# Performance work log

Hardware: AMD Instinct MI355X
Metric: run time of the kernel (lower is better)

The kernel has to match this reference:

```python
import jax, jax.numpy as jnp
import numpy as np

D_MODEL = 1024
N_HEADS = 16
HEAD_DIM = D_MODEL // N_HEADS
EPS = 1e-6


def _phi(x):
    # elu(x) + 1 feature map
    return jax.nn.elu(x) + 1.0


def setup_inputs() -> dict:
    key = jax.random.key(0)
    ks = jax.random.split(key, 12)
    B, N, M = 4, 4096, 4096
    s = 1.0 / np.sqrt(D_MODEL)
    return {
        "queries": jax.random.normal(ks[0], (B, N, D_MODEL), jnp.float32),
        "keys": jax.random.normal(ks[1], (B, M, D_MODEL), jnp.float32),
        "values": jax.random.normal(ks[2], (B, M, D_MODEL), jnp.float32),
        "wq": jax.random.normal(ks[3], (D_MODEL, D_MODEL), jnp.float32) * s,
        "bq": jax.random.normal(ks[4], (D_MODEL,), jnp.float32) * s,
        "wk": jax.random.normal(ks[5], (D_MODEL, D_MODEL), jnp.float32) * s,
        "bk": jax.random.normal(ks[6], (D_MODEL,), jnp.float32) * s,
        "wv": jax.random.normal(ks[7], (D_MODEL, D_MODEL), jnp.float32) * s,
        "bv": jax.random.normal(ks[8], (D_MODEL,), jnp.float32) * s,
        "wo": jax.random.normal(ks[9], (D_MODEL, D_MODEL), jnp.float32) * s,
        "bo": jax.random.normal(ks[10], (D_MODEL,), jnp.float32) * s,
    }


def reference(queries, keys, values, wq, bq, wk, bk, wv, bv, wo, bo):
    B, N, _ = queries.shape
    M = keys.shape[1]
    H, Dh = N_HEADS, HEAD_DIM
    # projections + head split -> [B, H, seq, Dh]
    q = _phi((queries @ wq.T + bq).reshape(B, N, H, Dh).transpose(0, 2, 1, 3))
    k = _phi((keys @ wk.T + bk).reshape(B, M, H, Dh).transpose(0, 2, 1, 3))
    v = (values @ wv.T + bv).reshape(B, M, H, Dh).transpose(0, 2, 1, 3)
    # kv aggregation: [B,H,Dh,Dh]
    kv = jnp.einsum("bhmd,bhme->bhde", k, v)
    # normalizer: [B,H,Dh]
    z = k.sum(axis=2)
    num = jnp.einsum("bhnd,bhde->bhne", q, kv)
    den = jnp.einsum("bhnd,bhd->bhn", q, z)[..., None] + EPS
    out = (num / den).transpose(0, 2, 1, 3).reshape(B, N, H * Dh)
    return out @ wo.T + bo
```

## Files before the change

### kernel.cpp

```cpp
#include <hip/hip_runtime.h>

#define EPS 1e-6f

typedef __attribute__((ext_vector_type(8))) __bf16 bf16x8;
typedef __attribute__((ext_vector_type(4))) float f32x4;
typedef __attribute__((ext_vector_type(4))) unsigned short us4v;
typedef __attribute__((ext_vector_type(8))) unsigned short us8v;
typedef unsigned short us;

__device__ inline us f2bf(float f) {
  unsigned int u = __builtin_bit_cast(unsigned int, f);
  unsigned int r = (u + 0x7fffu + ((u >> 16) & 1u)) >> 16;
  return (us)r;
}
__device__ inline float bf2f(us s) {
  unsigned int u = ((unsigned int)s) << 16;
  return __builtin_bit_cast(float, u);
}

__device__ inline void gl_lds16(const us* g, us* l) {
  __builtin_amdgcn_global_load_lds(
      (const __attribute__((address_space(1))) unsigned int*)g,
      (__attribute__((address_space(3))) unsigned int*)l, 16, 0, 0);
}

__global__ __launch_bounds__(256) void conv_bf16(const float* __restrict__ s,
                                                 us* __restrict__ d) {
  int idx = blockIdx.x * 256 + threadIdx.x;
  size_t base = (size_t)idx * 8;
  float4 a = *(const float4*)(s + base);
  float4 b = *(const float4*)(s + base + 4);
  us8v o;
  o[0] = f2bf(a.x); o[1] = f2bf(a.y); o[2] = f2bf(a.z); o[3] = f2bf(a.w);
  o[4] = f2bf(b.x); o[5] = f2bf(b.y); o[6] = f2bf(b.z); o[7] = f2bf(b.w);
  *(us8v*)(d + base) = o;
}

__global__ __launch_bounds__(256) void conv_w4(const float* __restrict__ wq,
                                               const float* __restrict__ wk,
                                               const float* __restrict__ wv,
                                               const float* __restrict__ wo,
                                               us* __restrict__ dq,
                                               us* __restrict__ dk,
                                               us* __restrict__ dv,
                                               us* __restrict__ dwo) {
  int bid = blockIdx.x;
  int msel = bid >> 9, lb = bid & 511;
  const float* s = (msel == 0) ? wq : (msel == 1) ? wk : (msel == 2) ? wv : wo;
  us* d = (msel == 0) ? dq : (msel == 1) ? dk : (msel == 2) ? dv : dwo;
  int idx = lb * 256 + threadIdx.x;
  size_t base = (size_t)idx * 8;
  float4 a = *(const float4*)(s + base);
  float4 b = *(const float4*)(s + base + 4);
  us8v o;
  o[0] = f2bf(a.x); o[1] = f2bf(a.y); o[2] = f2bf(a.z); o[3] = f2bf(a.w);
  o[4] = f2bf(b.x); o[5] = f2bf(b.y); o[6] = f2bf(b.z); o[7] = f2bf(b.w);
  *(us8v*)(d + base) = o;
}

template <int MODE>
__global__ __launch_bounds__(512, 2) void proj_gemm(const us* __restrict__ X,
                                                    const us* __restrict__ W,
                                                    const float* __restrict__ bias,
                                                    void* __restrict__ Yv) {
  __shared__ alignas(16) us As[2][256 * 64];
  __shared__ alignas(16) us Bs[2][256 * 64];

  const int t = threadIdx.x;
  const int wave = t >> 6, lane = t & 63;
  const int q4 = lane >> 4, l16 = lane & 15;
  const int wm = wave >> 2, wn = wave & 3;
  const int bid = blockIdx.x;
  const int rowg = (bid & 7) * 8 + (bid >> 5);
  const int colg = (bid >> 3) & 3;
  const int rowBase = rowg << 8;
  const int colBase = colg << 8;

  const int tr = t >> 3;
  const int gsw = ((t & 7) ^ (tr & 7)) * 8;
  const us* Xg = X + (size_t)(rowBase + tr) * 1024 + gsw;
  const us* Wg = W + (size_t)(colBase + tr) * 1024 + gsw;

  const int gx0 = ((0 | q4) ^ (l16 & 7)) * 8;
  const int gx1 = ((4 | q4) ^ (l16 & 7)) * 8;
  const int arow_off = (wm * 128 + l16) * 64;
  const int brow_off = (wn * 64 + l16) * 64;

  f32x4 acc[8][4];
#pragma unroll
  for (int i = 0; i < 8; i++)
#pragma unroll
    for (int j = 0; j < 4; j++) acc[i][j] = (f32x4){0.f, 0.f, 0.f, 0.f};

#define STAGE_A(kt, h)                                                      \
  {                                                                         \
    us* d_ = &As[(kt) & 1][((h) * 128 + wave * 8) * 64];                    \
    const us* s_ = Xg + (size_t)((h) * 128) * 1024 + (kt) * 64;             \
    gl_lds16(s_, d_);                                                       \
    gl_lds16(s_ + (size_t)64 * 1024, d_ + 64 * 64);                         \
  }
#define STAGE_B(kt, h)                                                      \
  {                                                                         \
    us* d_ = &Bs[(kt) & 1][((h) * 128 + wave * 8) * 64];                    \
    const us* s_ = Wg + (size_t)((h) * 128) * 1024 + (kt) * 64;             \
    gl_lds16(s_, d_);                                                       \
    gl_lds16(s_ + (size_t)64 * 1024, d_ + 64 * 64);                         \
  }
#define PH_SYNC_PRE()                                                       \
  asm volatile("s_barrier" ::: "memory");                                   \
  asm volatile("s_waitcnt lgkmcnt(0)" ::: "memory");                        \
  __builtin_amdgcn_sched_barrier(0);                                        \
  __builtin_amdgcn_s_setprio(1);
#define PH_SYNC_POST()                                                      \
  __builtin_amdgcn_s_setprio(0);                                           \
  asm volatile("s_barrier" ::: "memory");
#define MFMA16(J, AF)                                                       \
  _Pragma("unroll") for (int s_i = 0; s_i < 2; ++s_i)                       \
  _Pragma("unroll") for (int ks = 0; ks < 2; ++ks)                          \
  _Pragma("unroll") for (int ni = 0; ni < 4; ++ni)                          \
    acc[2 * (J) + s_i][ni] = __builtin_amdgcn_mfma_f32_16x16x32_bf16(       \
        AF[s_i][ks], bfv[ni][ks], acc[2 * (J) + s_i][ni], 0, 0, 0);

  STAGE_B(0, 0); STAGE_B(0, 1);
  STAGE_A(0, 0); STAGE_A(0, 1);
  STAGE_B(1, 0); STAGE_B(1, 1);
  asm volatile("s_waitcnt vmcnt(4)" ::: "memory");
  asm volatile("s_barrier" ::: "memory");

#pragma unroll 2
  for (int m = 0; m < 16; ++m) {
    const int b = m & 1;
    const us* Ar = &As[b][arow_off];
    const us* Br = &Bs[b][brow_off];
    bf16x8 bfv[4][2];

    {
      bf16x8 af[2][2];
#pragma unroll
      for (int s_i = 0; s_i < 2; ++s_i) {
        af[s_i][0] = *(const bf16x8*)(Ar + (0 + s_i) * 1024 + gx0);
        af[s_i][1] = *(const bf16x8*)(Ar + (0 + s_i) * 1024 + gx1);
      }
#pragma unroll
      for (int ni = 0; ni < 4; ++ni) {
        bfv[ni][0] = *(const bf16x8*)(Br + ni * 1024 + gx0);
        bfv[ni][1] = *(const bf16x8*)(Br + ni * 1024 + gx1);
      }
      if (m < 15) STAGE_A(m + 1, 0);
      PH_SYNC_PRE();
      MFMA16(0, af);
      PH_SYNC_POST();
    }
    {
      bf16x8 af[2][2];
#pragma unroll
      for (int s_i = 0; s_i < 2; ++s_i) {
        af[s_i][0] = *(const bf16x8*)(Ar + (2 + s_i) * 1024 + gx0);
        af[s_i][1] = *(const bf16x8*)(Ar + (2 + s_i) * 1024 + gx1);
      }
      if (m < 15) STAGE_A(m + 1, 1);
      PH_SYNC_PRE();
      MFMA16(1, af);
      PH_SYNC_POST();
    }
    {
      bf16x8 af[2][2];
#pragma unroll
      for (int s_i = 0; s_i < 2; ++s_i) {
        af[s_i][0] = *(const bf16x8*)(Ar + (4 + s_i) * 1024 + gx0);
        af[s_i][1] = *(const bf16x8*)(Ar + (4 + s_i) * 1024 + gx1);
      }
      if (m < 14) STAGE_B(m + 2, 0);
      PH_SYNC_PRE();
      MFMA16(2, af);
      PH_SYNC_POST();
    }
    {
      bf16x8 af[2][2];
#pragma unroll
      for (int s_i = 0; s_i < 2; ++s_i) {
        af[s_i][0] = *(const bf16x8*)(Ar + (6 + s_i) * 1024 + gx0);
        af[s_i][1] = *(const bf16x8*)(Ar + (6 + s_i) * 1024 + gx1);
      }
      if (m < 14) STAGE_B(m + 2, 1);
      asm volatile("s_barrier" ::: "memory");
      asm volatile("s_waitcnt lgkmcnt(0)" ::: "memory");
      __builtin_amdgcn_sched_barrier(0);
      __builtin_amdgcn_s_setprio(1);
      MFMA16(3, af);
      __builtin_amdgcn_s_setprio(0);
      if (m < 14)
        asm volatile("s_waitcnt vmcnt(4)" ::: "memory");
      else
        asm volatile("s_waitcnt vmcnt(0)" ::: "memory");
      asm volatile("s_barrier" ::: "memory");
    }
  }
#undef STAGE_A
#undef STAGE_B
#undef PH_SYNC_PRE
#undef PH_SYNC_POST
#undef MFMA16

#pragma unroll
  for (int j = 0; j < 4; j++) {
    int col = colBase + wn * 64 + j * 16 + l16;
    float bv = bias[col];
#pragma unroll
    for (int i = 0; i < 8; i++) {
      int row0 = rowBase + wm * 128 + i * 16 + q4 * 4;
      if (MODE == 1 || MODE == 2) {
        int bb = row0 >> 12, m0 = row0 & 4095;
        int h = col >> 6, dd = col & 63;
        us4v pk;
#pragma unroll
        for (int r = 0; r < 4; r++) {
          float y = acc[i][j][r] + bv;
          if (MODE == 1) y = (y > 0.f) ? (y + 1.f) : __expf(y);
          pk[r] = f2bf(y);
        }
        *(us4v*)&((us*)Yv)[(((size_t)((bb * 16 + h) * 64 + dd)) << 12) + m0] = pk;
      } else {
#pragma unroll
        for (int r = 0; r < 4; r++) {
          float y = acc[i][j][r] + bv;
          if (MODE == 0) {
            y = (y > 0.f) ? (y + 1.f) : __expf(y);
            ((us*)Yv)[(size_t)(row0 + r) * 1024 + col] = f2bf(y);
          } else {
            ((float*)Yv)[(size_t)(row0 + r) * 1024 + col] = y;
          }
        }
      }
    }
  }
}

__global__ __launch_bounds__(256) void kv_stage1(const us* __restrict__ kt,
                                                 const us* __restrict__ vt,
                                                 float* __restrict__ part,
                                                 float* __restrict__ zpart) {
  __shared__ float red[4][4096];
  __shared__ float zred[4][64][4];

  const int blk = blockIdx.x;
  const int bh = blk & 63, split = blk >> 6;
  const int t = threadIdx.x;
  const int w = t >> 6, lane = t & 63;
  const int q4 = lane >> 4, l16 = lane & 15;
  const us* ktb = kt + (size_t)bh * 64 * 4096;
  const us* vtb = vt + (size_t)bh * 64 * 4096;
  const int mbeg = split * 512 + w * 128;

  f32x4 acc[4][4];
#pragma unroll
  for (int i = 0; i < 4; i++)
#pragma unroll
    for (int j = 0; j < 4; j++) acc[i][j] = (f32x4){0.f, 0.f, 0.f, 0.f};
  float zacc[4] = {0.f, 0.f, 0.f, 0.f};

  us8v ka[4], va[4], kb[4], vb[4];
#define LOADF(K, V, m0)                                                       \
  _Pragma("unroll") for (int i = 0; i < 4; ++i) {                             \
    V[i] = *(const us8v*)&vtb[(size_t)(i * 16 + l16) * 4096 + (m0) + q4 * 8]; \
    K[i] = *(const us8v*)&ktb[(size_t)(i * 16 + l16) * 4096 + (m0) + q4 * 8]; \
  }
#define STEPF(K, V)                                                           \
  {                                                                           \
    bf16x8 af[4], bfr[4];                                                     \
    _Pragma("unroll") for (int j = 0; j < 4; ++j) {                           \
      bfr[j] = __builtin_bit_cast(bf16x8, K[j]);                              \
      _Pragma("unroll") for (int e = 0; e < 8; ++e) zacc[j] += bf2f(K[j][e]); \
    }                                                                         \
    _Pragma("unroll") for (int i = 0; i < 4; ++i)                             \
      af[i] = __builtin_bit_cast(bf16x8, V[i]);                               \
    _Pragma("unroll") for (int i = 0; i < 4; ++i)                             \
      _Pragma("unroll") for (int j = 0; j < 4; ++j)                           \
        acc[i][j] = __builtin_amdgcn_mfma_f32_16x16x32_bf16(                  \
            af[i], bfr[j], acc[i][j], 0, 0, 0);                               \
  }

  LOADF(ka, va, mbeg);
  LOADF(kb, vb, mbeg + 32);
  STEPF(ka, va);
  LOADF(ka, va, mbeg + 64);
  STEPF(kb, vb);
  LOADF(kb, vb, mbeg + 96);
  STEPF(ka, va);
  STEPF(kb, vb);
#undef LOADF
#undef STEPF

#pragma unroll
  for (int i = 0; i < 4; i++)
#pragma unroll
    for (int j = 0; j < 4; j++)
#pragma unroll
      for (int r = 0; r < 4; r++)
        red[w][(i * 16 + q4 * 4 + r) * 64 + j * 16 + l16] = acc[i][j][r];
#pragma unroll
  for (int j = 0; j < 4; j++) zred[w][j * 16 + l16][q4] = zacc[j];
  __syncthreads();

  float* pb = part + (size_t)blk * 4096;
#pragma unroll
  for (int i = 0; i < 16; i++) {
    int idx = t + 256 * i;
    pb[idx] = red[0][idx] + red[1][idx] + red[2][idx] + red[3][idx];
  }
  if (t < 64) {
    float s = 0.f;
#pragma unroll
    for (int w2 = 0; w2 < 4; w2++)
#pragma unroll
      for (int q = 0; q < 4; q++) s += zred[w2][t][q];
    zpart[blk * 64 + t] = s;
  }
}

__global__ __launch_bounds__(256) void kv_stage2(const float* __restrict__ part,
                                                 const float* __restrict__ zpart,
                                                 us* __restrict__ kvb,
                                                 float* __restrict__ z) {
  const int bh = blockIdx.x;
  const int t = threadIdx.x;
  const float* p0 = part + (size_t)bh * 4096;
#pragma unroll
  for (int i = 0; i < 16; i++) {
    int idx = t + 256 * i;
    float s = 0.f;
#pragma unroll
    for (int sp = 0; sp < 8; sp++) s += p0[(size_t)sp * 262144 + idx];
    kvb[(size_t)bh * 4096 + idx] = f2bf(s);
  }
  if (t < 64) {
    const float* zp = zpart + bh * 64;
    float s = 0.f;
#pragma unroll
    for (int sp = 0; sp < 8; sp++) s += zp[sp * 4096 + t];
    z[bh * 64 + t] = s;
  }
}

__global__ __launch_bounds__(256) void attn_kernel(const us* __restrict__ q,
                                                   const us* __restrict__ kvb,
                                                   const float* __restrict__ z,
                                                   us* __restrict__ attn) {
  __shared__ alignas(16) us kvs[64 * 72];
  __shared__ float zs[64];
  __shared__ float invden[256];

  const int bid = blockIdx.x;
  const int bh = bid >> 4, nc = bid & 15;
  const int b = bh >> 4, h = bh & 15;
  const int n0 = nc * 256;
  const int t = threadIdx.x;
  const int wave = t >> 6, lane = t & 63;
  const int q4 = lane >> 4, l16 = lane & 15;

#pragma unroll
  for (int i = 0; i < 2; i++) {
    int chunk = t + 256 * i;
    int e = chunk >> 3, d8 = chunk & 7;
    us8v vv = *(const us8v*)&kvb[(size_t)bh * 4096 + chunk * 8];
    *(us8v*)&kvs[e * 72 + d8 * 8] = vv;
  }
  if (t < 64) zs[t] = z[bh * 64 + t];
  __syncthreads();

  {
    const us* qrow = q + ((size_t)(b * 4096 + n0 + t)) * 1024 + h * 64;
    float s = 0.f;
#pragma unroll
    for (int d0 = 0; d0 < 64; d0 += 8) {
      us8v v = *(const us8v*)(qrow + d0);
#pragma unroll
      for (int j = 0; j < 8; j++) s += bf2f(v[j]) * zs[d0 + j];
    }
    invden[t] = 1.0f / (s + EPS);
  }
  __syncthreads();

  f32x4 acc[4][4];
#pragma unroll
  for (int i = 0; i < 4; i++)
#pragma unroll
    for (int j = 0; j < 4; j++) acc[i][j] = (f32x4){0.f, 0.f, 0.f, 0.f};

  const us* qb = q + ((size_t)(b * 4096 + n0 + wave * 64)) * 1024 + h * 64;
#pragma unroll
  for (int ks = 0; ks < 2; ks++) {
    bf16x8 af[4], bfr[4];
#pragma unroll
    for (int i = 0; i < 4; i++)
      af[i] = *(const bf16x8*)(qb + (size_t)(i * 16 + l16) * 1024 + ks * 32 + q4 * 8);
#pragma unroll
    for (int j = 0; j < 4; j++)
      bfr[j] = *(const bf16x8*)&kvs[(j * 16 + l16) * 72 + ks * 32 + q4 * 8];
#pragma unroll
    for (int i = 0; i < 4; i++)
#pragma unroll
      for (int j = 0; j < 4; j++)
        acc[i][j] = __builtin_amdgcn_mfma_f32_16x16x32_bf16(af[i], bfr[j], acc[i][j], 0, 0, 0);
  }

  us* ab = attn + ((size_t)(b * 4096 + n0 + wave * 64)) * 1024 + h * 64;
#pragma unroll
  for (int i = 0; i < 4; i++)
#pragma unroll
    for (int j = 0; j < 4; j++)
#pragma unroll
      for (int r = 0; r < 4; r++) {
        int rowl = i * 16 + q4 * 4 + r;
        int nl = wave * 64 + rowl;
        int e = j * 16 + l16;
        ab[(size_t)rowl * 1024 + e] = f2bf(acc[i][j][r] * invden[nl]);
      }
}

extern "C" void kernel_launch(void* const* d_in, const int* in_sizes, int n_in,
                              void* d_out, int out_size, void* d_ws, size_t ws_size,
                              hipStream_t stream) {
  const float* queries = (const float*)d_in[0];
  const float* keys    = (const float*)d_in[1];
  const float* values  = (const float*)d_in[2];
  const float* wq = (const float*)d_in[3];
  const float* bq = (const float*)d_in[4];
  const float* wk = (const float*)d_in[5];
  const float* bk = (const float*)d_in[6];
  const float* wv = (const float*)d_in[7];
  const float* bv = (const float*)d_in[8];
  const float* wo = (const float*)d_in[9];
  const float* bo = (const float*)d_in[10];

  char* ws = (char*)d_ws;
  const size_t TB = (size_t)16384 * 1024 * 2;
  us* A   = (us*)(ws);
  us* Bb  = (us*)(ws + TB);
  us* Xb  = (us*)(ws + 2 * TB);
  us* wqb = (us*)(ws + 3 * TB);
  us* wkb = wqb + (size_t)1024 * 1024;
  us* wvb = wkb + (size_t)1024 * 1024;
  us* wob = wvb + (size_t)1024 * 1024;
  float* z   = (float*)(wob + (size_t)1024 * 1024);
  us* kvb    = (us*)(z + 4096);
  float* part  = (float*)Xb;
  float* zpart = part + (size_t)512 * 4096;

  const int GRID_IN = 16384 * 1024 / 2048;

  conv_w4<<<2048, 256, 0, stream>>>(wq, wk, wv, wo, wqb, wkb, wvb, wob);

  conv_bf16<<<GRID_IN, 256, 0, stream>>>(keys, Xb);
  proj_gemm<1><<<256, 512, 0, stream>>>(Xb, wkb, bk, (void*)A);
  conv_bf16<<<GRID_IN, 256, 0, stream>>>(values, Xb);
  proj_gemm<2><<<256, 512, 0, stream>>>(Xb, wvb, bv, (void*)Bb);
  kv_stage1<<<512, 256, 0, stream>>>(A, Bb, part, zpart);
  kv_stage2<<<64, 256, 0, stream>>>(part, zpart, kvb, z);
  conv_bf16<<<GRID_IN, 256, 0, stream>>>(queries, Bb);
  proj_gemm<0><<<256, 512, 0, stream>>>(Bb, wqb, bq, (void*)A);
  attn_kernel<<<1024, 256, 0, stream>>>(A, kvb, z, A);
  proj_gemm<3><<<256, 512, 0, stream>>>(A, wob, bo, d_out);
}
```

Before: 435.1 us.

## Stage GEMM and attention epilogues through swizzled LDS for coalesced stores

The bf16 epilogues of the projection GEMM (modes 0/1/2) and the attention kernel now write results into a transposed, XOR-swizzled LDS tile, then read them back so that global stores are contiguous vector writes. Before, each lane stored scattered 2-byte or 8-byte elements with large strides. The double-buffer arrays are merged into one shared buffer so the epilogue can reuse that LDS, and each epilogue gains a barrier. The transpose reads gather single elements from LDS, which may cause bank conflicts that offset part of the gain in store efficiency.

```diff
diff --git a/kernel.cpp b/kernel.cpp
--- a/kernel.cpp
+++ b/kernel.cpp
@@ -23,6 +23,8 @@
       (const __attribute__((address_space(1))) unsigned int*)g,
       (__attribute__((address_space(3))) unsigned int*)l, 16, 0, 0);
 }
+
+#define EMASK(lc) (((((lc) & 15) ^ (((lc) >> 4) & 3)) << 2))
 
 __global__ __launch_bounds__(256) void conv_bf16(const float* __restrict__ s,
                                                  us* __restrict__ d) {
@@ -63,8 +65,11 @@
                                                     const us* __restrict__ W,
                                                     const float* __restrict__ bias,
                                                     void* __restrict__ Yv) {
-  __shared__ alignas(16) us As[2][256 * 64];
-  __shared__ alignas(16) us Bs[2][256 * 64];
+  __shared__ alignas(16) us SH[65536];
+  us* As0 = SH;
+  us* As1 = SH + 16384;
+  us* Bs0 = SH + 32768;
+  us* Bs1 = SH + 49152;
 
   const int t = threadIdx.x;
   const int wave = t >> 6, lane = t & 63;
@@ -94,14 +99,14 @@
 
 #define STAGE_A(kt, h)                                                      \
   {                                                                         \
-    us* d_ = &As[(kt) & 1][((h) * 128 + wave * 8) * 64];                    \
+    us* d_ = ((kt) & 1 ? As1 : As0) + ((h) * 128 + wave * 8) * 64;          \
     const us* s_ = Xg + (size_t)((h) * 128) * 1024 + (kt) * 64;             \
     gl_lds16(s_, d_);                                                       \
     gl_lds16(s_ + (size_t)64 * 1024, d_ + 64 * 64);                         \
   }
 #define STAGE_B(kt, h)                                                      \
   {                                                                         \
-    us* d_ = &Bs[(kt) & 1][((h) * 128 + wave * 8) * 64];                    \
+    us* d_ = ((kt) & 1 ? Bs1 : Bs0) + ((h) * 128 + wave * 8) * 64;          \
     const us* s_ = Wg + (size_t)((h) * 128) * 1024 + (kt) * 64;             \
     gl_lds16(s_, d_);                                                       \
     gl_lds16(s_ + (size_t)64 * 1024, d_ + 64 * 64);                         \
@@ -130,8 +135,8 @@
 #pragma unroll 2
   for (int m = 0; m < 16; ++m) {
     const int b = m & 1;
-    const us* Ar = &As[b][arow_off];
-    const us* Br = &Bs[b][brow_off];
+    const us* Ar = (b ? As1 : As0) + arow_off;
+    const us* Br = (b ? Bs1 : Bs0) + brow_off;
     bf16x8 bfv[4][2];
 
     {
@@ -202,35 +207,63 @@
 #undef PH_SYNC_POST
 #undef MFMA16
 
-#pragma unroll
-  for (int j = 0; j < 4; j++) {
-    int col = colBase + wn * 64 + j * 16 + l16;
-    float bv = bias[col];
-#pragma unroll
-    for (int i = 0; i < 8; i++) {
-      int row0 = rowBase + wm * 128 + i * 16 + q4 * 4;
-      if (MODE == 1 || MODE == 2) {
-        int bb = row0 >> 12, m0 = row0 & 4095;
-        int h = col >> 6, dd = col & 63;
+  if (MODE == 3) {
+#pragma unroll
+    for (int j = 0; j < 4; j++) {
+      int col = colBase + wn * 64 + j * 16 + l16;
+      float bv = bias[col];
+#pragma unroll
+      for (int i = 0; i < 8; i++) {
+        int row0 = rowBase + wm * 128 + i * 16 + q4 * 4;
+#pragma unroll
+        for (int r = 0; r < 4; r++)
+          ((float*)Yv)[(size_t)(row0 + r) * 1024 + col] = acc[i][j][r] + bv;
+      }
+    }
+  } else {
+    us* T = SH;
+#pragma unroll
+    for (int j = 0; j < 4; j++) {
+      int lc = wn * 64 + j * 16 + l16;
+      float bv = bias[colBase + lc];
+#pragma unroll
+      for (int i = 0; i < 8; i++) {
+        int lr0 = wm * 128 + i * 16 + q4 * 4;
         us4v pk;
 #pragma unroll
         for (int r = 0; r < 4; r++) {
           float y = acc[i][j][r] + bv;
-          if (MODE == 1) y = (y > 0.f) ? (y + 1.f) : __expf(y);
+          if (MODE != 2) y = (y > 0.f) ? (y + 1.f) : __expf(y);
           pk[r] = f2bf(y);
         }
-        *(us4v*)&((us*)Yv)[(((size_t)((bb * 16 + h) * 64 + dd)) << 12) + m0] = pk;
-      } else {
-#pragma unroll
-        for (int r = 0; r < 4; r++) {
-          float y = acc[i][j][r] + bv;
-          if (MODE == 0) {
-            y = (y > 0.f) ? (y + 1.f) : __expf(y);
-            ((us*)Yv)[(size_t)(row0 + r) * 1024 + col] = f2bf(y);
-          } else {
-            ((float*)Yv)[(size_t)(row0 + r) * 1024 + col] = y;
-          }
+        *(us4v*)&T[lc * 256 + (lr0 ^ EMASK(lc))] = pk;
+      }
+    }
+    __syncthreads();
+
+    if (MODE == 1 || MODE == 2) {
+      const int bb = rowBase >> 12, m0 = rowBase & 4095;
+#pragma unroll
+      for (int kk = 0; kk < 32; kk++) {
+        int lc = wave + 8 * kk;
+        int gcol = colBase + lc;
+        int h = gcol >> 6, dd = gcol & 63;
+        us4v v = *(const us4v*)&T[lc * 256 + ((lane * 4) ^ EMASK(lc))];
+        *(us4v*)&((us*)Yv)[(((size_t)((bb * 16 + h) * 64 + dd)) << 12) + m0 +
+                           lane * 4] = v;
+      }
+    } else {
+#pragma unroll
+      for (int kk = 0; kk < 32; kk++) {
+        int lr = wave + 8 * kk;
+        us4v v;
+#pragma unroll
+        for (int d = 0; d < 4; d++) {
+          int lc = lane * 4 + d;
+          v[d] = T[lc * 256 + (lr ^ EMASK(lc))];
         }
+        *(us4v*)&((us*)Yv)[(size_t)(rowBase + lr) * 1024 + colBase +
+                           lane * 4] = v;
       }
     }
   }
@@ -346,9 +379,11 @@
                                                    const us* __restrict__ kvb,
                                                    const float* __restrict__ z,
                                                    us* __restrict__ attn) {
-  __shared__ alignas(16) us kvs[64 * 72];
+  __shared__ alignas(16) us SH2[16384];
   __shared__ float zs[64];
   __shared__ float invden[256];
+
+  us* kvs = SH2;
 
   const int bid = blockIdx.x;
   const int bh = bid >> 4, nc = bid & 15;
@@ -404,18 +439,35 @@
         acc[i][j] = __builtin_amdgcn_mfma_f32_16x16x32_bf16(af[i], bfr[j], acc[i][j], 0, 0, 0);
   }
 
-  us* ab = attn + ((size_t)(b * 4096 + n0 + wave * 64)) * 1024 + h * 64;
+  __syncthreads();
+  us* T2 = SH2;
 #pragma unroll
   for (int i = 0; i < 4; i++)
 #pragma unroll
-    for (int j = 0; j < 4; j++)
-#pragma unroll
-      for (int r = 0; r < 4; r++) {
-        int rowl = i * 16 + q4 * 4 + r;
-        int nl = wave * 64 + rowl;
-        int e = j * 16 + l16;
-        ab[(size_t)rowl * 1024 + e] = f2bf(acc[i][j][r] * invden[nl]);
-      }
+    for (int j = 0; j < 4; j++) {
+      int e = j * 16 + l16;
+      int nl0 = wave * 64 + i * 16 + q4 * 4;
+      us4v pk;
+#pragma unroll
+      for (int r = 0; r < 4; r++)
+        pk[r] = f2bf(acc[i][j][r] * invden[nl0 + r]);
+      *(us4v*)&T2[e * 256 + (nl0 ^ EMASK(e))] = pk;
+    }
+  __syncthreads();
+
+  us* ob = attn + ((size_t)(b * 4096 + n0)) * 1024 + h * 64;
+#pragma unroll
+  for (int pass = 0; pass < 8; pass++) {
+    int n = pass * 32 + (t >> 3);
+    int e0 = (t & 7) * 8;
+    us8v v;
+#pragma unroll
+    for (int d = 0; d < 8; d++) {
+      int e = e0 + d;
+      v[d] = T2[e * 256 + (n ^ EMASK(e))];
+    }
+    *(us8v*)&ob[(size_t)n * 1024 + e0] = v;
+  }
 }
 
 extern "C" void kernel_launch(void* const* d_in, const int* in_sizes, int n_in,
```

New measurement: 429.3 us. About the same (-1.3%).
